# Performance work log

Hardware: AMD Instinct MI355X
Metric: run time of the kernel (lower is better)

## Reference

```python
import jax, jax.numpy as jnp
import numpy as np

N_GENES = 15135
K = int(np.ceil(0.5 * N_GENES))  # 7568, PyG TopKPooling ratio=0.5
BS, E, F_IN, H, HF, NC, L = 8, 242160, 64, 128, 512, 2, 3


def setup_inputs() -> dict:
    key = jax.random.key(0)
    ks = jax.random.split(key, 16)
    def lin(k, fin, fout):
        s = 1.0 / np.sqrt(fin)
        return jax.random.normal(k, (fin, fout), jnp.float32) * s
    x = jax.random.normal(ks[0], (BS, N_GENES, F_IN), jnp.float32)
    batch = jnp.zeros((BS,), jnp.int32)
    edge_index = jax.random.randint(ks[1], (2, E), 0, N_GENES, dtype=jnp.int32)
    CAT = L * H
    return {
        "x": x,
        "batch": batch,
        "edge_index": edge_index,
        "W1": lin(ks[2], F_IN, H), "b1": jnp.zeros((H,), jnp.float32),
        "W2": lin(ks[3], H, H),    "b2": jnp.zeros((H,), jnp.float32),
        "W3": lin(ks[4], H, H),    "b3": jnp.zeros((H,), jnp.float32),
        "topk_w": jax.random.normal(ks[5], (CAT,), jnp.float32) / np.sqrt(CAT),
        "fcW": lin(ks[6], CAT, 1), "fcb": jnp.zeros((1,), jnp.float32),
        "lin1W": lin(ks[7], K, HF), "lin1b": jnp.zeros((HF,), jnp.float32),
        "lin2W": lin(ks[8], HF, NC), "lin2b": jnp.zeros((NC,), jnp.float32),
    }


def reference(x, batch, edge_index, W1, b1, W2, b2, W3, b3,
              topk_w, fcW, fcb, lin1W, lin1b, lin2W, lin2b):
    bs = x.shape[0]
    # --- GCN normalization with self-loops (PyG GCNConv defaults) ---
    loop = jnp.arange(N_GENES, dtype=edge_index.dtype)
    src = jnp.concatenate([edge_index[0], loop])
    dst = jnp.concatenate([edge_index[1], loop])
    deg = jnp.zeros((N_GENES,), x.dtype).at[dst].add(1.0)
    dinv = jax.lax.rsqrt(deg)  # deg >= 1 due to self-loops
    norm = dinv[src] * dinv[dst]  # [E+N]

    def gcn(h, W, b):
        h = h @ W                                   # [bs, N, H]
        msg = h[:, src, :] * norm[None, :, None]    # gather + edge weight
        agg = jnp.zeros_like(h).at[:, dst, :].add(msg)  # scatter-add
        return agg + b

    h1 = jax.nn.relu(gcn(x, W1, b1))
    h2 = jax.nn.relu(gcn(h1, W2, b2))
    h3 = jax.nn.relu(gcn(h2, W3, b3))
    # mode='cat': stack on last dim then flatten -> feature order (H, layer)
    xc = jnp.stack([h1, h2, h3], -1).reshape(bs, N_GENES, -1)  # [bs, N, L*H]

    # --- TopKPooling (score = tanh(x.w/||w||), keep top ceil(0.5*N)) ---
    score = jnp.tanh((xc @ topk_w) / jnp.linalg.norm(topk_w))  # [bs, N]
    top_s, perm = jax.lax.top_k(score, K)                       # [bs, K]
    xp = jnp.take_along_axis(xc, perm[..., None], axis=1) * top_s[..., None]

    z = (xp @ fcW + fcb)[..., 0]          # [bs, K]
    h = jax.nn.relu(z @ lin1W + lin1b)    # [bs, HF]; dropout inactive (eval)
    logits = h @ lin2W + lin2b            # [bs, NC]
    return jax.nn.log_softmax(logits, axis=-1)
```

## Files before the change

kernel.cpp:

```cpp
#include <hip/hip_runtime.h>

#define N_G   15135
#define E_N   242160
#define BSZ   8
#define K_TOP 7568
#define NH    128
#define NBIN  65536
#define SUFS  65600

typedef float f4v __attribute__((ext_vector_type(4)));
typedef float f2v __attribute__((ext_vector_type(2)));

__global__ void zero_kernel(int* __restrict__ p, int n) {
  int i = blockIdx.x * 1024 + threadIdx.x;
  if (i < n) p[i] = 0;
}

__global__ void count_kernel(const int* __restrict__ ei, int* __restrict__ cnt) {
  int e = blockIdx.x * 256 + threadIdx.x;
  if (e < E_N) atomicAdd(&cnt[ei[E_N + e]], 1);
}

__global__ __launch_bounds__(1024) void scan_kernel(const int* __restrict__ cnt,
                                                    int* __restrict__ rowstart,
                                                    float* __restrict__ dinv,
                                                    int4* __restrict__ rowdesc,
                                                    int* __restrict__ gctr,
                                                    const float* __restrict__ topk_w,
                                                    float* __restrict__ scal) {
  __shared__ int buf[1024];
  __shared__ int base;
  int tid = threadIdx.x;
  int i = blockIdx.x * 1024 + tid;
  int v = (i < N_G) ? cnt[i] : 0;
  float di = 1.0f / sqrtf((float)(v + 1));
  if (i < N_G) dinv[i] = di;
  buf[tid] = v;
  __syncthreads();
  for (int s = 1; s < 1024; s <<= 1) {
    int t = (tid >= s) ? buf[tid - s] : 0;
    __syncthreads();
    buf[tid] += t;
    __syncthreads();
  }
  if (tid == 1023) base = atomicAdd(gctr, buf[1023]);
  __syncthreads();
  if (i < N_G) {
    int rs = base + buf[tid] - v;
    rowstart[i] = rs;
    rowdesc[i] = make_int4(rs, v, __float_as_int(di), 0);
  }
  if (blockIdx.x == 0) {
    __shared__ float fbuf[512];
    if (tid < 512) {
      float w = (tid < 384) ? topk_w[tid] : 0.f;
      fbuf[tid] = w * w;
    }
    __syncthreads();
    for (int s = 256; s > 0; s >>= 1) {
      if (tid < s) fbuf[tid] += fbuf[tid + s];
      __syncthreads();
    }
    if (tid == 0) scal[0] = 1.0f / sqrtf(fbuf[0]);
  }
}

__global__ void fill_kernel(const int* __restrict__ ei, const int* __restrict__ rowstart,
                            const float* __restrict__ dinv, int* __restrict__ fillc,
                            int2* __restrict__ csr) {
  int e = blockIdx.x * 256 + threadIdx.x;
  if (e < E_N) {
    int s = ei[e], d = ei[E_N + e];
    int pos = rowstart[d] + atomicAdd(&fillc[d], 1);
    csr[pos] = make_int2(s, __float_as_int(dinv[s]));
  }
}

template<int CIN, bool BR>
__global__ __launch_bounds__(256, 6) void mm_kernel(const float* __restrict__ A,
                                                    const float* __restrict__ W,
                                                    const float* __restrict__ bias,
                                                    float* __restrict__ out) {
  __shared__ float Bst[32][132];
  __shared__ float Ast2[32][68];
  int tid = threadIdx.x;
  int b = blockIdx.x & 7;
  int ib = blockIdx.x >> 3;
  int rb0 = b * N_G + ib * 64;
  int rmax = N_G - ib * 64;
  int c0 = (tid & 31) * 4;
  int r0 = (tid >> 5) * 8;
  float acc[8][4];
#pragma unroll
  for (int i = 0; i < 8; i++)
#pragma unroll
    for (int j = 0; j < 4; j++) acc[i][j] = 0.f;

  for (int k0 = 0; k0 < CIN; k0 += 32) {
    {
      int koff = (tid & 7) * 4;
      int row = tid >> 3;
#pragma unroll
      for (int p = 0; p < 2; ++p) {
        int r = row + p * 32;
        f4v v = {0.f, 0.f, 0.f, 0.f};
        if (r < rmax) v = __builtin_nontemporal_load((const f4v*)(A + (size_t)(rb0 + r) * CIN + k0 + koff));
        Ast2[koff + 0][r] = v.x; Ast2[koff + 1][r] = v.y;
        Ast2[koff + 2][r] = v.z; Ast2[koff + 3][r] = v.w;
      }
    }
    {
      int cc = (tid & 31) * 4;
      int kr = tid >> 5;
#pragma unroll
      for (int p = 0; p < 4; ++p) {
        int k = kr + p * 8;
        *(float4*)&Bst[k][cc] = *(const float4*)(W + (size_t)(k0 + k) * NH + cc);
      }
    }
    __syncthreads();
#pragma unroll 4
    for (int kk = 0; kk < 32; ++kk) {
      float a[8], bb[4];
      *(float4*)&a[0] = *(const float4*)&Ast2[kk][r0];
      *(float4*)&a[4] = *(const float4*)&Ast2[kk][r0 + 4];
      *(float4*)&bb[0] = *(const float4*)&Bst[kk][c0];
#pragma unroll
      for (int i = 0; i < 8; i++)
#pragma unroll
        for (int j = 0; j < 4; j++)
          acc[i][j] = fmaf(a[i], bb[j], acc[i][j]);
    }
    __syncthreads();
  }
  float b0 = 0.f, b1 = 0.f, b2 = 0.f, b3 = 0.f;
  if (BR) { b0 = bias[c0]; b1 = bias[c0+1]; b2 = bias[c0+2]; b3 = bias[c0+3]; }
#pragma unroll
  for (int i = 0; i < 8; i++) {
    int r = r0 + i;
    if (r < rmax) {
      float4 v;
      if (BR) {
        v.x = fmaxf(acc[i][0] + b0, 0.f); v.y = fmaxf(acc[i][1] + b1, 0.f);
        v.z = fmaxf(acc[i][2] + b2, 0.f); v.w = fmaxf(acc[i][3] + b3, 0.f);
      } else {
        v.x = acc[i][0]; v.y = acc[i][1]; v.z = acc[i][2]; v.w = acc[i][3];
      }
      *(float4*)(out + (size_t)(rb0 + r) * NH + c0) = v;
    }
  }
}

__global__ __launch_bounds__(256) void agg64_kernel(const float* __restrict__ src,
                                                    const int2* __restrict__ csr,
                                                    const int4* __restrict__ rowdesc,
                                                    float* __restrict__ dst) {
  int b = blockIdx.x & 7;
  int chunk = blockIdx.x >> 3;
  int wave = threadIdx.x >> 6, lane = threadIdx.x & 63;
  int d = chunk * 4 + wave;
  if (d >= N_G) return;
  d = __builtin_amdgcn_readfirstlane(d);
  int4 rd = rowdesc[d];
  int e0 = rd.x, n = rd.y;
  float dv = __int_as_float(rd.z);
  const float* sb = src + (size_t)b * N_G * 64;
  const int2* ce = csr + e0;
  float acc[8];
  acc[0] = dv * sb[(size_t)d * 64 + lane];
#pragma unroll
  for (int k = 1; k < 8; ++k) acc[k] = 0.f;
  int l = 0;
  if (n >= 8) {
    int2 pA[8]; float vA[8];
#pragma unroll
    for (int k = 0; k < 8; ++k) pA[k] = ce[k];
#pragma unroll
    for (int k = 0; k < 8; ++k) vA[k] = sb[(size_t)pA[k].x * 64 + lane];
    l = 8;
    for (; l + 8 <= n; l += 8) {
      int2 pB[8]; float vB[8];
#pragma unroll
      for (int k = 0; k < 8; ++k) pB[k] = ce[l + k];
#pragma unroll
      for (int k = 0; k < 8; ++k) vB[k] = sb[(size_t)pB[k].x * 64 + lane];
#pragma unroll
      for (int k = 0; k < 8; ++k) acc[k] = fmaf(__int_as_float(pA[k].y), vA[k], acc[k]);
#pragma unroll
      for (int k = 0; k < 8; ++k) { pA[k] = pB[k]; vA[k] = vB[k]; }
    }
#pragma unroll
    for (int k = 0; k < 8; ++k) acc[k] = fmaf(__int_as_float(pA[k].y), vA[k], acc[k]);
  }
  for (; l < n; ++l) {
    int2 p = ce[l];
    acc[0] = fmaf(__int_as_float(p.y), sb[(size_t)p.x * 64 + lane], acc[0]);
  }
  float s = ((acc[0] + acc[1]) + (acc[2] + acc[3])) + ((acc[4] + acc[5]) + (acc[6] + acc[7]));
  __builtin_nontemporal_store(dv * s, &dst[((size_t)b * N_G + d) * 64 + lane]);
}

template<int CH0>
__global__ __launch_bounds__(256) void agg_h_kernel(const float* __restrict__ hw,
                                                    const int2* __restrict__ csr,
                                                    const int4* __restrict__ rowdesc,
                                                    const float* __restrict__ bias,
                                                    float* __restrict__ hout) {
  int b = blockIdx.x & 7;
  int chunk = blockIdx.x >> 3;
  int wave = threadIdx.x >> 6, lane = threadIdx.x & 63;
  int d0 = chunk * 8 + wave * 2;
  if (d0 >= N_G) return;
  d0 = __builtin_amdgcn_readfirstlane(d0);
  int d1i = d0 + 1;
  int has1 = (d1i < N_G);
  int dB = has1 ? d1i : d0;
  int4 rdA = rowdesc[d0];
  int4 rdB = rowdesc[dB];
  int nA = rdA.y, nB = has1 ? rdB.y : 0;
  float dvA = __int_as_float(rdA.z);
  float dvB = __int_as_float(rdB.z);
  const float* sb = hw + (size_t)b * N_G * NH + CH0 + lane;
  const int2* ceA = csr + rdA.x;
  const int2* ceB = csr + rdB.x;
  float axA[4], axB[4];
  axA[0] = dvA * sb[(size_t)d0 * NH];
  axB[0] = has1 ? dvB * sb[(size_t)dB * NH] : 0.f;
#pragma unroll
  for (int k = 1; k < 4; ++k) { axA[k] = 0.f; axB[k] = 0.f; }
  int lA = 0, lB = 0;
  while (lA + 8 <= nA && lB + 8 <= nB) {
    int2 pA[8], pB[8]; float vA[8], vB[8];
#pragma unroll
    for (int k = 0; k < 8; ++k) pA[k] = ceA[lA + k];
#pragma unroll
    for (int k = 0; k < 8; ++k) pB[k] = ceB[lB + k];
#pragma unroll
    for (int k = 0; k < 8; ++k) vA[k] = sb[(size_t)pA[k].x * NH];
#pragma unroll
    for (int k = 0; k < 8; ++k) vB[k] = sb[(size_t)pB[k].x * NH];
#pragma unroll
    for (int k = 0; k < 8; ++k) axA[k & 3] = fmaf(__int_as_float(pA[k].y), vA[k], axA[k & 3]);
#pragma unroll
    for (int k = 0; k < 8; ++k) axB[k & 3] = fmaf(__int_as_float(pB[k].y), vB[k], axB[k & 3]);
    lA += 8; lB += 8;
  }
  for (; lA + 8 <= nA; lA += 8) {
    int2 pA[8]; float vA[8];
#pragma unroll
    for (int k = 0; k < 8; ++k) pA[k] = ceA[lA + k];
#pragma unroll
    for (int k = 0; k < 8; ++k) vA[k] = sb[(size_t)pA[k].x * NH];
#pragma unroll
    for (int k = 0; k < 8; ++k) axA[k & 3] = fmaf(__int_as_float(pA[k].y), vA[k], axA[k & 3]);
  }
  for (; lB + 8 <= nB; lB += 8) {
    int2 pB[8]; float vB[8];
#pragma unroll
    for (int k = 0; k < 8; ++k) pB[k] = ceB[lB + k];
#pragma unroll
    for (int k = 0; k < 8; ++k) vB[k] = sb[(size_t)pB[k].x * NH];
#pragma unroll
    for (int k = 0; k < 8; ++k) axB[k & 3] = fmaf(__int_as_float(pB[k].y), vB[k], axB[k & 3]);
  }
  for (; lA < nA; ++lA) {
    int2 p = ceA[lA];
    axA[0] = fmaf(__int_as_float(p.y), sb[(size_t)p.x * NH], axA[0]);
  }
  for (; lB < nB; ++lB) {
    int2 p = ceB[lB];
    axB[0] = fmaf(__int_as_float(p.y), sb[(size_t)p.x * NH], axB[0]);
  }
  float bb = bias[CH0 + lane];
  {
    float s = (axA[0] + axA[1]) + (axA[2] + axA[3]);
    __builtin_nontemporal_store(fmaxf(fmaf(dvA, s, bb), 0.f),
        &hout[((size_t)b * N_G + d0) * NH + CH0 + lane]);
  }
  if (has1) {
    float s = (axB[0] + axB[1]) + (axB[2] + axB[3]);
    __builtin_nontemporal_store(fmaxf(fmaf(dvB, s, bb), 0.f),
        &hout[((size_t)b * N_G + d1i) * NH + CH0 + lane]);
  }
}

template<int CH0, bool FINAL>
__global__ __launch_bounds__(256) void agg_score_h_kernel(const float* __restrict__ hw,
                                                          const int2* __restrict__ csr,
                                                          const int4* __restrict__ rowdesc,
                                                          const float* __restrict__ bias,
                                                          const float* __restrict__ h1,
                                                          const float* __restrict__ h2,
                                                          const float* __restrict__ topk_w,
                                                          const float* __restrict__ fcW,
                                                          const float* __restrict__ scal,
                                                          float* __restrict__ score,
                                                          float* __restrict__ d2a,
                                                          unsigned* __restrict__ keys,
                                                          int* __restrict__ hist,
                                                          float2* __restrict__ dpart) {
  int b = blockIdx.x & 7;
  int chunk = blockIdx.x >> 3;
  int wave = threadIdx.x >> 6, lane = threadIdx.x & 63;
  int d0 = chunk * 8 + wave * 2;
  if (d0 >= N_G) return;
  d0 = __builtin_amdgcn_readfirstlane(d0);
  int d1i = d0 + 1;
  int has1 = (d1i < N_G);
  int dB = has1 ? d1i : d0;
  int4 rdA = rowdesc[d0];
  int4 rdB = rowdesc[dB];
  int nA = rdA.y, nB = has1 ? rdB.y : 0;
  float dvA = __int_as_float(rdA.z);
  float dvB = __int_as_float(rdB.z);
  const float* sb = hw + (size_t)b * N_G * NH + CH0 + lane;
  const int2* ceA = csr + rdA.x;
  const int2* ceB = csr + rdB.x;
  size_t rbA = ((size_t)b * N_G + d0) * NH + CH0 + lane;
  size_t rbB = ((size_t)b * N_G + dB) * NH + CH0 + lane;
  float u1A = __builtin_nontemporal_load(&h1[rbA]);
  float u2A = __builtin_nontemporal_load(&h2[rbA]);
  float u1B = __builtin_nontemporal_load(&h1[rbB]);
  float u2B = __builtin_nontemporal_load(&h2[rbB]);
  float axA[4], axB[4];
  axA[0] = dvA * sb[(size_t)d0 * NH];
  axB[0] = has1 ? dvB * sb[(size_t)dB * NH] : 0.f;
#pragma unroll
  for (int k = 1; k < 4; ++k) { axA[k] = 0.f; axB[k] = 0.f; }
  int lA = 0, lB = 0;
  while (lA + 8 <= nA && lB + 8 <= nB) {
    int2 pA[8], pB[8]; float vA[8], vB[8];
#pragma unroll
    for (int k = 0; k < 8; ++k) pA[k] = ceA[lA + k];
#pragma unroll
    for (int k = 0; k < 8; ++k) pB[k] = ceB[lB + k];
#pragma unroll
    for (int k = 0; k < 8; ++k) vA[k] = sb[(size_t)pA[k].x * NH];
#pragma unroll
    for (int k = 0; k < 8; ++k) vB[k] = sb[(size_t)pB[k].x * NH];
#pragma unroll
    for (int k = 0; k < 8; ++k) axA[k & 3] = fmaf(__int_as_float(pA[k].y), vA[k], axA[k & 3]);
#pragma unroll
    for (int k = 0; k < 8; ++k) axB[k & 3] = fmaf(__int_as_float(pB[k].y), vB[k], axB[k & 3]);
    lA += 8; lB += 8;
  }
  for (; lA + 8 <= nA; lA += 8) {
    int2 pA[8]; float vA[8];
#pragma unroll
    for (int k = 0; k < 8; ++k) pA[k] = ceA[lA + k];
#pragma unroll
    for (int k = 0; k < 8; ++k) vA[k] = sb[(size_t)pA[k].x * NH];
#pragma unroll
    for (int k = 0; k < 8; ++k) axA[k & 3] = fmaf(__int_as_float(pA[k].y), vA[k], axA[k & 3]);
  }
  for (; lB + 8 <= nB; lB += 8) {
    int2 pB[8]; float vB[8];
#pragma unroll
    for (int k = 0; k < 8; ++k) pB[k] = ceB[lB + k];
#pragma unroll
    for (int k = 0; k < 8; ++k) vB[k] = sb[(size_t)pB[k].x * NH];
#pragma unroll
    for (int k = 0; k < 8; ++k) axB[k & 3] = fmaf(__int_as_float(pB[k].y), vB[k], axB[k & 3]);
  }
  for (; lA < nA; ++lA) {
    int2 p = ceA[lA];
    axA[0] = fmaf(__int_as_float(p.y), sb[(size_t)p.x * NH], axA[0]);
  }
  for (; lB < nB; ++lB) {
    int2 p = ceB[lB];
    axB[0] = fmaf(__int_as_float(p.y), sb[(size_t)p.x * NH], axB[0]);
  }
  float bb = bias[CH0 + lane];
  float rA = fmaxf(fmaf(dvA, (axA[0] + axA[1]) + (axA[2] + axA[3]), bb), 0.f);
  float rB = fmaxf(fmaf(dvB, (axB[0] + axB[1]) + (axB[2] + axB[3]), bb), 0.f);
  int ch3 = (CH0 + lane) * 3;
  float t0 = topk_w[ch3 + 0], t1 = topk_w[ch3 + 1], t2 = topk_w[ch3 + 2];
  float f0 = fcW[ch3 + 0],  f1 = fcW[ch3 + 1],  f2 = fcW[ch3 + 2];
  float d1A = u1A * t0 + u2A * t1 + rA * t2;
  float d2A = u1A * f0 + u2A * f1 + rA * f2;
  float d1B = u1B * t0 + u2B * t1 + rB * t2;
  float d2B = u1B * f0 + u2B * f1 + rB * f2;
#pragma unroll
  for (int sh = 32; sh > 0; sh >>= 1) {
    d1A += __shfl_down(d1A, sh);
    d2A += __shfl_down(d2A, sh);
    d1B += __shfl_down(d1B, sh);
    d2B += __shfl_down(d2B, sh);
  }
  if (lane == 0) {
    int gwA = b * N_G + d0;
    if (!FINAL) {
      dpart[gwA] = make_float2(d1A, d2A);
      if (has1) dpart[gwA + 1] = make_float2(d1B, d2B);
    } else {
      float sc0 = scal[0];
      {
        float2 pp = dpart[gwA];
        float D1 = pp.x + d1A, D2 = pp.y + d2A;
        float sc = tanhf(D1 * sc0);
        score[gwA] = sc;
        d2a[gwA] = D2;
        unsigned u = __float_as_uint(sc);
        unsigned k32 = (u & 0x80000000u) ? ~u : (u | 0x80000000u);
        keys[gwA] = k32;
        atomicAdd(&hist[b * NBIN + (int)(k32 >> 16)], 1);
      }
      if (has1) {
        int gwB = gwA + 1;
        float2 pp = dpart[gwB];
        float D1 = pp.x + d1B, D2 = pp.y + d2B;
        float sc = tanhf(D1 * sc0);
        score[gwB] = sc;
        d2a[gwB] = D2;
        unsigned u = __float_as_uint(sc);
        unsigned k32 = (u & 0x80000000u) ? ~u : (u | 0x80000000u);
        keys[gwB] = k32;
        atomicAdd(&hist[b * NBIN + (int)(k32 >> 16)], 1);
      }
    }
  }
}

__global__ __launch_bounds__(1024) void suffix_kernel(const int* __restrict__ hist,
                                                      int* __restrict__ suf) {
  __shared__ int buf[1024];
  int b = blockIdx.x;
  const int* hb = hist + b * NBIN;
  int* sb = suf + b * SUFS;
  int t = threadIdx.x;
  int base = t * 64;
  int s = 0;
  for (int k = 0; k < 64; ++k) s += hb[base + k];
  buf[t] = s;
  __syncthreads();
  for (int off = 1; off < 1024; off <<= 1) {
    int v = (t + off < 1024) ? buf[t + off] : 0;
    __syncthreads();
    buf[t] += v;
    __syncthreads();
  }
  int acc = buf[t] - s;
  if (t == 0) sb[NBIN] = 0;
  for (int k = 63; k >= 0; --k) {
    acc += hb[base + k];
    sb[base + k] = acc;
  }
}

__global__ void scatter_kernel(const unsigned* __restrict__ keys, int* __restrict__ hist,
                               const int* __restrict__ suf, int2* __restrict__ bucket) {
  int b = blockIdx.y;
  int i = blockIdx.x * 256 + threadIdx.x;
  if (i >= N_G) return;
  unsigned k = keys[b * N_G + i];
  int bin = (int)(k >> 16);
  int old = atomicSub(&hist[b * NBIN + bin], 1);
  int pos = suf[b * SUFS + bin + 1] + old - 1;
  bucket[b * N_G + pos] = make_int2((int)k, i);
}

__global__ void rank_z_kernel(const unsigned* __restrict__ keys, const int* __restrict__ suf,
                              const int2* __restrict__ bucket, const float* __restrict__ score,
                              const float* __restrict__ d2a, const float* __restrict__ fcb,
                              float* __restrict__ z) {
  int b = blockIdx.y;
  int i = blockIdx.x * 256 + threadIdx.x;
  if (i >= N_G) return;
  int gw = b * N_G + i;
  unsigned k = keys[gw];
  int bin = (int)(k >> 16);
  int lo = suf[b * SUFS + bin + 1];
  int hi = suf[b * SUFS + bin];
  int r = lo;
  const int2* bk = bucket + b * N_G;
  for (int p = lo; p < hi; ++p) {
    int2 e = bk[p];
    unsigned kj = (unsigned)e.x;
    r += (kj > k || (kj == k && e.y < i)) ? 1 : 0;
  }
  if (r < K_TOP) z[b * K_TOP + r] = fmaf(score[gw], d2a[gw], fcb[0]);
}

__global__ __launch_bounds__(256) void lin1_kernel(const float* __restrict__ z,
                                                   const float* __restrict__ W,
                                                   float* __restrict__ hpre) {
  __shared__ float zb[237];
  int b = blockIdx.y, rs = blockIdx.x;
  int r0 = rs * 237;
  int rn = K_TOP - r0; if (rn > 237) rn = 237;
  for (int q = threadIdx.x; q < rn; q += 256) zb[q] = z[b * K_TOP + r0 + q];
  __syncthreads();
  int c = threadIdx.x;
  float a0 = 0.f, a1 = 0.f;
  for (int r = 0; r < rn; ++r) {
    float zz = zb[r];
    const float* wr = W + (size_t)(r0 + r) * 512;
    a0 = fmaf(zz, wr[c], a0);
    a1 = fmaf(zz, wr[c + 256], a1);
  }
  atomicAdd(&hpre[b * 512 + c], a0);
  atomicAdd(&hpre[b * 512 + c + 256], a1);
}

__global__ __launch_bounds__(128) void lin2_kernel(const float* __restrict__ hpre,
                                                   const float* __restrict__ l1b,
                                                   const float* __restrict__ W2,
                                                   const float* __restrict__ l2b,
                                                   float* __restrict__ out) {
  int b = blockIdx.x, tid = threadIdx.x;
  float a0 = 0.f, a1 = 0.f;
  for (int j = tid; j < 512; j += 128) {
    float t = fmaxf(hpre[b * 512 + j] + l1b[j], 0.f);
    a0 = fmaf(t, W2[j * 2 + 0], a0);
    a1 = fmaf(t, W2[j * 2 + 1], a1);
  }
#pragma unroll
  for (int s = 32; s > 0; s >>= 1) {
    a0 += __shfl_down(a0, s);
    a1 += __shfl_down(a1, s);
  }
  __shared__ float red[2][2];
  if ((tid & 63) == 0) { red[tid >> 6][0] = a0; red[tid >> 6][1] = a1; }
  __syncthreads();
  if (tid == 0) {
    float l0 = red[0][0] + red[1][0] + l2b[0];
    float l1 = red[0][1] + red[1][1] + l2b[1];
    float m = fmaxf(l0, l1);
    float lse = m + logf(expf(l0 - m) + expf(l1 - m));
    out[b * 2 + 0] = l0 - lse;
    out[b * 2 + 1] = l1 - lse;
  }
}

extern "C" void kernel_launch(void* const* d_in, const int* in_sizes, int n_in,
                              void* d_out, int out_size, void* d_ws, size_t ws_size,
                              hipStream_t stream) {
  const float* x   = (const float*)d_in[0];
  const int*   ei  = (const int*)d_in[2];
  const float* W1  = (const float*)d_in[3];
  const float* b1  = (const float*)d_in[4];
  const float* W2  = (const float*)d_in[5];
  const float* b2  = (const float*)d_in[6];
  const float* W3  = (const float*)d_in[7];
  const float* b3  = (const float*)d_in[8];
  const float* tkw = (const float*)d_in[9];
  const float* fcW = (const float*)d_in[10];
  const float* fcb = (const float*)d_in[11];
  const float* l1W = (const float*)d_in[12];
  const float* l1b = (const float*)d_in[13];
  const float* l2W = (const float*)d_in[14];
  const float* l2b = (const float*)d_in[15];
  float* out = (float*)d_out;

  char* ws = (char*)d_ws;
  size_t off = 0;
  auto alloc = [&](size_t bytes) {
    char* p = ws + off;
    off += (bytes + 255) & ~(size_t)255;
    return p;
  };
  int*   cnt   = (int*)alloc(15136 * 4);
  int*   fillc = (int*)alloc(15136 * 4);
  int*   gctr  = (int*)alloc(256);
  float* hpre  = (float*)alloc(4096 * 4);
  int*   hist  = (int*)alloc((size_t)BSZ * NBIN * 4);
  int*   rowstart = (int*)alloc(15136 * 4);
  float* dinv  = (float*)alloc(15136 * 4);
  int4*  rowdesc = (int4*)alloc(15136 * 16);
  float* scal  = (float*)alloc(64);
  float* z     = (float*)alloc((size_t)BSZ * K_TOP * 4);
  float* score = (float*)alloc(121088 * 4);
  float* d2a   = (float*)alloc(121088 * 4);
  unsigned* keys = (unsigned*)alloc(121088 * 4);
  int*   suf   = (int*)alloc((size_t)BSZ * SUFS * 4);
  int2*  bucket = (int2*)alloc(121088 * 8);
  int2*  csr   = (int2*)alloc((size_t)E_N * 8);
  float* ax = (float*)alloc((size_t)BSZ * N_G * 64 * 4);
  float* hw = (float*)alloc((size_t)BSZ * N_G * NH * 4);
  float* h1 = (float*)alloc((size_t)BSZ * N_G * NH * 4);
  float* h2 = (float*)alloc((size_t)BSZ * N_G * NH * 4);
  (void)ws_size; (void)in_sizes; (void)n_in; (void)out_size;

  float2* dpart = (float2*)bucket;

  int zero_n = (int)(((char*)rowstart - (char*)cnt) / 4);
  zero_kernel<<<(zero_n + 1023) / 1024, 1024, 0, stream>>>(cnt, zero_n);
  count_kernel<<<(E_N + 255) / 256, 256, 0, stream>>>(ei, cnt);
  scan_kernel<<<(N_G + 1023) / 1024, 1024, 0, stream>>>(cnt, rowstart, dinv, rowdesc, gctr, tkw, scal);
  fill_kernel<<<(E_N + 255) / 256, 256, 0, stream>>>(ei, rowstart, dinv, fillc, csr);

  dim3 mmg(8 * 237);
  int aggblocks  = 8 * ((N_G + 3) / 4);
  int aggblocks2 = 8 * ((N_G + 7) / 8);

  agg64_kernel<<<aggblocks, 256, 0, stream>>>(x, csr, rowdesc, ax);
  mm_kernel<64, true><<<mmg, 256, 0, stream>>>(ax, W1, b1, h1);
  mm_kernel<128, false><<<mmg, 256, 0, stream>>>(h1, W2, nullptr, hw);
  agg_h_kernel<0><<<aggblocks2, 256, 0, stream>>>(hw, csr, rowdesc, b2, h2);
  agg_h_kernel<64><<<aggblocks2, 256, 0, stream>>>(hw, csr, rowdesc, b2, h2);
  mm_kernel<128, false><<<mmg, 256, 0, stream>>>(h2, W3, nullptr, hw);
  agg_score_h_kernel<0, false><<<aggblocks2, 256, 0, stream>>>(hw, csr, rowdesc, b3, h1, h2,
                                                               tkw, fcW, scal, score, d2a,
                                                               keys, hist, dpart);
  agg_score_h_kernel<64, true><<<aggblocks2, 256, 0, stream>>>(hw, csr, rowdesc, b3, h1, h2,
                                                               tkw, fcW, scal, score, d2a,
                                                               keys, hist, dpart);

  dim3 ng((N_G + 255) / 256, BSZ);
  suffix_kernel<<<BSZ, 1024, 0, stream>>>(hist, suf);
  scatter_kernel<<<ng, 256, 0, stream>>>(keys, hist, suf, bucket);
  rank_z_kernel<<<ng, 256, 0, stream>>>(keys, suf, bucket, score, d2a, fcb, z);

  dim3 l1g(32, BSZ);
  lin1_kernel<<<l1g, 256, 0, stream>>>(z, l1W, hpre);
  lin2_kernel<<<BSZ, 128, 0, stream>>>(hpre, l1b, l2W, l2b, out);
}
```

Measured before the change: 638.7 us.

## Replace per-row gather kernels with edge-streaming multi-row aggregation kernel

Replaces the three aggregation kernels, which gave each wave one or two destination rows, with one templated kernel. In it each wave walks the contiguous CSR edge range of 32 consecutive rows and finalizes each row when the edge index crosses its bound. The aim is to remove load imbalance and tail inefficiency from short or uneven row degrees, and to keep an 8-deep prefetch pipeline of edges and gathered values running across row boundaries. The trade-offs are serialized finalize logic per row inside the wave, fewer waves in total (about 474 per batch), and scalar bound-checking inside the inner loop, which may reduce parallelism and latency hiding.

```diff
diff --git a/kernel.cpp b/kernel.cpp
--- a/kernel.cpp
+++ b/kernel.cpp
@@ -10,6 +10,7 @@
 
 typedef float f4v __attribute__((ext_vector_type(4)));
 typedef float f2v __attribute__((ext_vector_type(2)));
+typedef int   i2v __attribute__((ext_vector_type(2)));
 
 __global__ void zero_kernel(int* __restrict__ p, int n) {
   int i = blockIdx.x * 1024 + threadIdx.x;
@@ -151,273 +152,181 @@
   }
 }
 
-__global__ __launch_bounds__(256) void agg64_kernel(const float* __restrict__ src,
-                                                    const int2* __restrict__ csr,
-                                                    const int4* __restrict__ rowdesc,
-                                                    float* __restrict__ dst) {
+template<int NHS, int CH0, int MODE>
+__global__ __launch_bounds__(256) void stream_agg_kernel(
+    const float* __restrict__ table,
+    const int2* __restrict__ csr,
+    const int4* __restrict__ rowdesc,
+    const float* __restrict__ bias,
+    const float* __restrict__ h1,
+    const float* __restrict__ h2,
+    const float* __restrict__ topk_w,
+    const float* __restrict__ fcW,
+    const float* __restrict__ scal,
+    float* __restrict__ outp,
+    float2* __restrict__ dpart,
+    float* __restrict__ score,
+    float* __restrict__ d2a,
+    unsigned* __restrict__ keys,
+    int* __restrict__ hist) {
+  constexpr int R = 32;
   int b = blockIdx.x & 7;
-  int chunk = blockIdx.x >> 3;
-  int wave = threadIdx.x >> 6, lane = threadIdx.x & 63;
-  int d = chunk * 4 + wave;
-  if (d >= N_G) return;
-  d = __builtin_amdgcn_readfirstlane(d);
-  int4 rd = rowdesc[d];
-  int e0 = rd.x, n = rd.y;
-  float dv = __int_as_float(rd.z);
-  const float* sb = src + (size_t)b * N_G * 64;
-  const int2* ce = csr + e0;
-  float acc[8];
-  acc[0] = dv * sb[(size_t)d * 64 + lane];
-#pragma unroll
-  for (int k = 1; k < 8; ++k) acc[k] = 0.f;
-  int l = 0;
-  if (n >= 8) {
-    int2 pA[8]; float vA[8];
-#pragma unroll
-    for (int k = 0; k < 8; ++k) pA[k] = ce[k];
-#pragma unroll
-    for (int k = 0; k < 8; ++k) vA[k] = sb[(size_t)pA[k].x * 64 + lane];
-    l = 8;
-    for (; l + 8 <= n; l += 8) {
-      int2 pB[8]; float vB[8];
-#pragma unroll
-      for (int k = 0; k < 8; ++k) pB[k] = ce[l + k];
-#pragma unroll
-      for (int k = 0; k < 8; ++k) vB[k] = sb[(size_t)pB[k].x * 64 + lane];
-#pragma unroll
-      for (int k = 0; k < 8; ++k) acc[k] = fmaf(__int_as_float(pA[k].y), vA[k], acc[k]);
-#pragma unroll
-      for (int k = 0; k < 8; ++k) { pA[k] = pB[k]; vA[k] = vB[k]; }
-    }
-#pragma unroll
-    for (int k = 0; k < 8; ++k) acc[k] = fmaf(__int_as_float(pA[k].y), vA[k], acc[k]);
-  }
-  for (; l < n; ++l) {
-    int2 p = ce[l];
-    acc[0] = fmaf(__int_as_float(p.y), sb[(size_t)p.x * 64 + lane], acc[0]);
-  }
-  float s = ((acc[0] + acc[1]) + (acc[2] + acc[3])) + ((acc[4] + acc[5]) + (acc[6] + acc[7]));
-  __builtin_nontemporal_store(dv * s, &dst[((size_t)b * N_G + d) * 64 + lane]);
-}
-
-template<int CH0>
-__global__ __launch_bounds__(256) void agg_h_kernel(const float* __restrict__ hw,
-                                                    const int2* __restrict__ csr,
-                                                    const int4* __restrict__ rowdesc,
-                                                    const float* __restrict__ bias,
-                                                    float* __restrict__ hout) {
-  int b = blockIdx.x & 7;
-  int chunk = blockIdx.x >> 3;
-  int wave = threadIdx.x >> 6, lane = threadIdx.x & 63;
-  int d0 = chunk * 8 + wave * 2;
+  int wid = (blockIdx.x >> 3) * 4 + (threadIdx.x >> 6);
+  int lane = threadIdx.x & 63;
+  int d0 = wid * R;
   if (d0 >= N_G) return;
   d0 = __builtin_amdgcn_readfirstlane(d0);
-  int d1i = d0 + 1;
-  int has1 = (d1i < N_G);
-  int dB = has1 ? d1i : d0;
-  int4 rdA = rowdesc[d0];
-  int4 rdB = rowdesc[dB];
-  int nA = rdA.y, nB = has1 ? rdB.y : 0;
-  float dvA = __int_as_float(rdA.z);
-  float dvB = __int_as_float(rdB.z);
-  const float* sb = hw + (size_t)b * N_G * NH + CH0 + lane;
-  const int2* ceA = csr + rdA.x;
-  const int2* ceB = csr + rdB.x;
-  float axA[4], axB[4];
-  axA[0] = dvA * sb[(size_t)d0 * NH];
-  axB[0] = has1 ? dvB * sb[(size_t)dB * NH] : 0.f;
-#pragma unroll
-  for (int k = 1; k < 4; ++k) { axA[k] = 0.f; axB[k] = 0.f; }
-  int lA = 0, lB = 0;
-  while (lA + 8 <= nA && lB + 8 <= nB) {
-    int2 pA[8], pB[8]; float vA[8], vB[8];
-#pragma unroll
-    for (int k = 0; k < 8; ++k) pA[k] = ceA[lA + k];
-#pragma unroll
-    for (int k = 0; k < 8; ++k) pB[k] = ceB[lB + k];
-#pragma unroll
-    for (int k = 0; k < 8; ++k) vA[k] = sb[(size_t)pA[k].x * NH];
-#pragma unroll
-    for (int k = 0; k < 8; ++k) vB[k] = sb[(size_t)pB[k].x * NH];
-#pragma unroll
-    for (int k = 0; k < 8; ++k) axA[k & 3] = fmaf(__int_as_float(pA[k].y), vA[k], axA[k & 3]);
-#pragma unroll
-    for (int k = 0; k < 8; ++k) axB[k & 3] = fmaf(__int_as_float(pB[k].y), vB[k], axB[k & 3]);
-    lA += 8; lB += 8;
-  }
-  for (; lA + 8 <= nA; lA += 8) {
-    int2 pA[8]; float vA[8];
-#pragma unroll
-    for (int k = 0; k < 8; ++k) pA[k] = ceA[lA + k];
-#pragma unroll
-    for (int k = 0; k < 8; ++k) vA[k] = sb[(size_t)pA[k].x * NH];
-#pragma unroll
-    for (int k = 0; k < 8; ++k) axA[k & 3] = fmaf(__int_as_float(pA[k].y), vA[k], axA[k & 3]);
-  }
-  for (; lB + 8 <= nB; lB += 8) {
-    int2 pB[8]; float vB[8];
-#pragma unroll
-    for (int k = 0; k < 8; ++k) pB[k] = ceB[lB + k];
-#pragma unroll
-    for (int k = 0; k < 8; ++k) vB[k] = sb[(size_t)pB[k].x * NH];
-#pragma unroll
-    for (int k = 0; k < 8; ++k) axB[k & 3] = fmaf(__int_as_float(pB[k].y), vB[k], axB[k & 3]);
-  }
-  for (; lA < nA; ++lA) {
-    int2 p = ceA[lA];
-    axA[0] = fmaf(__int_as_float(p.y), sb[(size_t)p.x * NH], axA[0]);
-  }
-  for (; lB < nB; ++lB) {
-    int2 p = ceB[lB];
-    axB[0] = fmaf(__int_as_float(p.y), sb[(size_t)p.x * NH], axB[0]);
-  }
-  float bb = bias[CH0 + lane];
-  {
-    float s = (axA[0] + axA[1]) + (axA[2] + axA[3]);
-    __builtin_nontemporal_store(fmaxf(fmaf(dvA, s, bb), 0.f),
-        &hout[((size_t)b * N_G + d0) * NH + CH0 + lane]);
-  }
-  if (has1) {
-    float s = (axB[0] + axB[1]) + (axB[2] + axB[3]);
-    __builtin_nontemporal_store(fmaxf(fmaf(dvB, s, bb), 0.f),
-        &hout[((size_t)b * N_G + d1i) * NH + CH0 + lane]);
-  }
-}
-
-template<int CH0, bool FINAL>
-__global__ __launch_bounds__(256) void agg_score_h_kernel(const float* __restrict__ hw,
-                                                          const int2* __restrict__ csr,
-                                                          const int4* __restrict__ rowdesc,
-                                                          const float* __restrict__ bias,
-                                                          const float* __restrict__ h1,
-                                                          const float* __restrict__ h2,
-                                                          const float* __restrict__ topk_w,
-                                                          const float* __restrict__ fcW,
-                                                          const float* __restrict__ scal,
-                                                          float* __restrict__ score,
-                                                          float* __restrict__ d2a,
-                                                          unsigned* __restrict__ keys,
-                                                          int* __restrict__ hist,
-                                                          float2* __restrict__ dpart) {
-  int b = blockIdx.x & 7;
-  int chunk = blockIdx.x >> 3;
-  int wave = threadIdx.x >> 6, lane = threadIdx.x & 63;
-  int d0 = chunk * 8 + wave * 2;
-  if (d0 >= N_G) return;
-  d0 = __builtin_amdgcn_readfirstlane(d0);
-  int d1i = d0 + 1;
-  int has1 = (d1i < N_G);
-  int dB = has1 ? d1i : d0;
-  int4 rdA = rowdesc[d0];
-  int4 rdB = rowdesc[dB];
-  int nA = rdA.y, nB = has1 ? rdB.y : 0;
-  float dvA = __int_as_float(rdA.z);
-  float dvB = __int_as_float(rdB.z);
-  const float* sb = hw + (size_t)b * N_G * NH + CH0 + lane;
-  const int2* ceA = csr + rdA.x;
-  const int2* ceB = csr + rdB.x;
-  size_t rbA = ((size_t)b * N_G + d0) * NH + CH0 + lane;
-  size_t rbB = ((size_t)b * N_G + dB) * NH + CH0 + lane;
-  float u1A = __builtin_nontemporal_load(&h1[rbA]);
-  float u2A = __builtin_nontemporal_load(&h2[rbA]);
-  float u1B = __builtin_nontemporal_load(&h1[rbB]);
-  float u2B = __builtin_nontemporal_load(&h2[rbB]);
-  float axA[4], axB[4];
-  axA[0] = dvA * sb[(size_t)d0 * NH];
-  axB[0] = has1 ? dvB * sb[(size_t)dB * NH] : 0.f;
-#pragma unroll
-  for (int k = 1; k < 4; ++k) { axA[k] = 0.f; axB[k] = 0.f; }
-  int lA = 0, lB = 0;
-  while (lA + 8 <= nA && lB + 8 <= nB) {
-    int2 pA[8], pB[8]; float vA[8], vB[8];
-#pragma unroll
-    for (int k = 0; k < 8; ++k) pA[k] = ceA[lA + k];
-#pragma unroll
-    for (int k = 0; k < 8; ++k) pB[k] = ceB[lB + k];
-#pragma unroll
-    for (int k = 0; k < 8; ++k) vA[k] = sb[(size_t)pA[k].x * NH];
-#pragma unroll
-    for (int k = 0; k < 8; ++k) vB[k] = sb[(size_t)pB[k].x * NH];
-#pragma unroll
-    for (int k = 0; k < 8; ++k) axA[k & 3] = fmaf(__int_as_float(pA[k].y), vA[k], axA[k & 3]);
-#pragma unroll
-    for (int k = 0; k < 8; ++k) axB[k & 3] = fmaf(__int_as_float(pB[k].y), vB[k], axB[k & 3]);
-    lA += 8; lB += 8;
-  }
-  for (; lA + 8 <= nA; lA += 8) {
-    int2 pA[8]; float vA[8];
-#pragma unroll
-    for (int k = 0; k < 8; ++k) pA[k] = ceA[lA + k];
-#pragma unroll
-    for (int k = 0; k < 8; ++k) vA[k] = sb[(size_t)pA[k].x * NH];
-#pragma unroll
-    for (int k = 0; k < 8; ++k) axA[k & 3] = fmaf(__int_as_float(pA[k].y), vA[k], axA[k & 3]);
-  }
-  for (; lB + 8 <= nB; lB += 8) {
-    int2 pB[8]; float vB[8];
-#pragma unroll
-    for (int k = 0; k < 8; ++k) pB[k] = ceB[lB + k];
-#pragma unroll
-    for (int k = 0; k < 8; ++k) vB[k] = sb[(size_t)pB[k].x * NH];
-#pragma unroll
-    for (int k = 0; k < 8; ++k) axB[k & 3] = fmaf(__int_as_float(pB[k].y), vB[k], axB[k & 3]);
-  }
-  for (; lA < nA; ++lA) {
-    int2 p = ceA[lA];
-    axA[0] = fmaf(__int_as_float(p.y), sb[(size_t)p.x * NH], axA[0]);
-  }
-  for (; lB < nB; ++lB) {
-    int2 p = ceB[lB];
-    axB[0] = fmaf(__int_as_float(p.y), sb[(size_t)p.x * NH], axB[0]);
-  }
-  float bb = bias[CH0 + lane];
-  float rA = fmaxf(fmaf(dvA, (axA[0] + axA[1]) + (axA[2] + axA[3]), bb), 0.f);
-  float rB = fmaxf(fmaf(dvB, (axB[0] + axB[1]) + (axB[2] + axB[3]), bb), 0.f);
-  int ch3 = (CH0 + lane) * 3;
-  float t0 = topk_w[ch3 + 0], t1 = topk_w[ch3 + 1], t2 = topk_w[ch3 + 2];
-  float f0 = fcW[ch3 + 0],  f1 = fcW[ch3 + 1],  f2 = fcW[ch3 + 2];
-  float d1A = u1A * t0 + u2A * t1 + rA * t2;
-  float d2A = u1A * f0 + u2A * f1 + rA * f2;
-  float d1B = u1B * t0 + u2B * t1 + rB * t2;
-  float d2B = u1B * f0 + u2B * f1 + rB * f2;
-#pragma unroll
-  for (int sh = 32; sh > 0; sh >>= 1) {
-    d1A += __shfl_down(d1A, sh);
-    d2A += __shfl_down(d2A, sh);
-    d1B += __shfl_down(d1B, sh);
-    d2B += __shfl_down(d2B, sh);
-  }
-  if (lane == 0) {
-    int gwA = b * N_G + d0;
-    if (!FINAL) {
-      dpart[gwA] = make_float2(d1A, d2A);
-      if (has1) dpart[gwA + 1] = make_float2(d1B, d2B);
+  int nrows = N_G - d0; if (nrows > R) nrows = R;
+
+  int rl = (lane < nrows) ? lane : (nrows - 1);
+  int4 rdl = rowdesc[d0 + rl];
+  int boundv = rdl.x + rdl.y;
+  float dinvv = __int_as_float(rdl.z);
+
+  const float* sb0 = table + (size_t)b * N_G * NHS + CH0;
+  const i2v* csrv = (const i2v*)csr;
+
+  int e    = __builtin_amdgcn_readfirstlane(__shfl(rdl.x, 0));
+  int eEnd = __builtin_amdgcn_readfirstlane(__shfl(boundv, nrows - 1));
+  int r = 0;
+  int bound = __builtin_amdgcn_readfirstlane(__shfl(boundv, 0));
+  float dv = __shfl(dinvv, 0);
+  float acc = 0.f;
+
+  float selfC, selfN;
+  selfC = sb0[(size_t)d0 * NHS + lane];
+  { int dn = d0 + 1; if (dn >= N_G) dn = N_G - 1; selfN = sb0[(size_t)dn * NHS + lane]; }
+
+  float bb = 0.f;
+  if constexpr (MODE >= 1) bb = bias[CH0 + lane];
+
+  float u1C = 0.f, u1N = 0.f, u2C = 0.f, u2N = 0.f;
+  float t0 = 0.f, t1 = 0.f, t2 = 0.f, f0 = 0.f, f1 = 0.f, f2 = 0.f;
+  float sc0 = 0.f;
+  float2 dpC = make_float2(0.f, 0.f), dpN = make_float2(0.f, 0.f);
+  if constexpr (MODE >= 2) {
+    size_t rb = ((size_t)b * N_G + d0) * NHS + CH0 + lane;
+    u1C = __builtin_nontemporal_load(&h1[rb]);
+    u2C = __builtin_nontemporal_load(&h2[rb]);
+    int dn = d0 + 1; if (dn >= N_G) dn = N_G - 1;
+    size_t rb1 = ((size_t)b * N_G + dn) * NHS + CH0 + lane;
+    u1N = __builtin_nontemporal_load(&h1[rb1]);
+    u2N = __builtin_nontemporal_load(&h2[rb1]);
+    int ch3 = (CH0 + lane) * 3;
+    t0 = topk_w[ch3]; t1 = topk_w[ch3 + 1]; t2 = topk_w[ch3 + 2];
+    f0 = fcW[ch3];    f1 = fcW[ch3 + 1];    f2 = fcW[ch3 + 2];
+  }
+  if constexpr (MODE == 3) {
+    sc0 = scal[0];
+    dpC = dpart[b * N_G + d0];
+    { int dn = d0 + 1; if (dn >= N_G) dn = N_G - 1; dpN = dpart[b * N_G + dn]; }
+  }
+
+  auto finalize = [&]() {
+    float s = acc + dv * selfC;
+    acc = 0.f;
+    int d = d0 + r;
+    selfC = selfN;
+    { int dn = d + 2; if (dn >= N_G) dn = N_G - 1; selfN = sb0[(size_t)dn * NHS + lane]; }
+    if constexpr (MODE == 0) {
+      __builtin_nontemporal_store(dv * s, &outp[((size_t)b * N_G + d) * NHS + CH0 + lane]);
+    } else if constexpr (MODE == 1) {
+      float rr = fmaxf(fmaf(dv, s, bb), 0.f);
+      __builtin_nontemporal_store(rr, &outp[((size_t)b * N_G + d) * NHS + CH0 + lane]);
     } else {
-      float sc0 = scal[0];
-      {
-        float2 pp = dpart[gwA];
-        float D1 = pp.x + d1A, D2 = pp.y + d2A;
-        float sc = tanhf(D1 * sc0);
-        score[gwA] = sc;
-        d2a[gwA] = D2;
-        unsigned u = __float_as_uint(sc);
-        unsigned k32 = (u & 0x80000000u) ? ~u : (u | 0x80000000u);
-        keys[gwA] = k32;
-        atomicAdd(&hist[b * NBIN + (int)(k32 >> 16)], 1);
-      }
-      if (has1) {
-        int gwB = gwA + 1;
-        float2 pp = dpart[gwB];
-        float D1 = pp.x + d1B, D2 = pp.y + d2B;
-        float sc = tanhf(D1 * sc0);
-        score[gwB] = sc;
-        d2a[gwB] = D2;
-        unsigned u = __float_as_uint(sc);
-        unsigned k32 = (u & 0x80000000u) ? ~u : (u | 0x80000000u);
-        keys[gwB] = k32;
-        atomicAdd(&hist[b * NBIN + (int)(k32 >> 16)], 1);
-      }
-    }
+      float rx = fmaxf(fmaf(dv, s, bb), 0.f);
+      float d1 = u1C * t0 + u2C * t1 + rx * t2;
+      float d2 = u1C * f0 + u2C * f1 + rx * f2;
+      u1C = u1N; u2C = u2N;
+      { int dn = d + 2; if (dn >= N_G) dn = N_G - 1;
+        size_t rb = ((size_t)b * N_G + dn) * NHS + CH0 + lane;
+        u1N = __builtin_nontemporal_load(&h1[rb]);
+        u2N = __builtin_nontemporal_load(&h2[rb]); }
+#pragma unroll
+      for (int sh = 32; sh > 0; sh >>= 1) {
+        d1 += __shfl_down(d1, sh);
+        d2 += __shfl_down(d2, sh);
+      }
+      int gw = b * N_G + d;
+      if constexpr (MODE == 2) {
+        if (lane == 0) dpart[gw] = make_float2(d1, d2);
+      } else {
+        float2 pp = dpC;
+        dpC = dpN;
+        { int dn = d + 2; if (dn >= N_G) dn = N_G - 1; dpN = dpart[b * N_G + dn]; }
+        if (lane == 0) {
+          float D1 = pp.x + d1, D2 = pp.y + d2;
+          float scv = tanhf(D1 * sc0);
+          score[gw] = scv;
+          d2a[gw] = D2;
+          unsigned u = __float_as_uint(scv);
+          unsigned k32 = (u & 0x80000000u) ? ~u : (u | 0x80000000u);
+          keys[gw] = k32;
+          atomicAdd(&hist[b * NBIN + (int)(k32 >> 16)], 1);
+        }
+      }
+    }
+  };
+
+  i2v csn[8];
+  float wC[8], vC[8];
+#pragma unroll
+  for (int k = 0; k < 8; ++k) {
+    int ei = e + k; if (ei > E_N - 1) ei = E_N - 1;
+    csn[k] = __builtin_nontemporal_load(&csrv[ei]);
+  }
+#pragma unroll
+  for (int k = 0; k < 8; ++k) {
+    int s = __builtin_amdgcn_readfirstlane(csn[k][0]);
+    wC[k] = __uint_as_float((unsigned)__builtin_amdgcn_readfirstlane(csn[k][1]));
+    vC[k] = sb0[(size_t)s * NHS + lane];
+  }
+#pragma unroll
+  for (int k = 0; k < 8; ++k) {
+    int ei = e + 8 + k; if (ei > E_N - 1) ei = E_N - 1;
+    csn[k] = __builtin_nontemporal_load(&csrv[ei]);
+  }
+
+  while (e < eEnd) {
+    bool more = (e + 8 < eEnd);
+    float wN[8], vN[8];
+    if (more) {
+#pragma unroll
+      for (int k = 0; k < 8; ++k) {
+        int s = __builtin_amdgcn_readfirstlane(csn[k][0]);
+        wN[k] = __uint_as_float((unsigned)__builtin_amdgcn_readfirstlane(csn[k][1]));
+        vN[k] = sb0[(size_t)s * NHS + lane];
+      }
+#pragma unroll
+      for (int k = 0; k < 8; ++k) {
+        int ei = e + 16 + k; if (ei > E_N - 1) ei = E_N - 1;
+        csn[k] = __builtin_nontemporal_load(&csrv[ei]);
+      }
+    }
+    int lim = eEnd - e; if (lim > 8) lim = 8;
+#pragma unroll
+    for (int k = 0; k < 8; ++k) {
+      if (k < lim) {
+        int eg = e + k;
+        while (eg == bound) {
+          finalize();
+          ++r;
+          int rr2 = (r < nrows) ? r : (nrows - 1);
+          bound = __builtin_amdgcn_readfirstlane(__shfl(boundv, rr2));
+          dv = __shfl(dinvv, rr2);
+        }
+        acc = fmaf(wC[k], vC[k], acc);
+      }
+    }
+#pragma unroll
+    for (int k = 0; k < 8; ++k) { wC[k] = wN[k]; vC[k] = vN[k]; }
+    e += 8;
+  }
+
+  while (r < nrows) {
+    dv = __shfl(dinvv, r);
+    finalize();
+    ++r;
   }
 }
 
@@ -590,21 +499,27 @@
   fill_kernel<<<(E_N + 255) / 256, 256, 0, stream>>>(ei, rowstart, dinv, fillc, csr);
 
   dim3 mmg(8 * 237);
-  int aggblocks  = 8 * ((N_G + 3) / 4);
-  int aggblocks2 = 8 * ((N_G + 7) / 8);
-
-  agg64_kernel<<<aggblocks, 256, 0, stream>>>(x, csr, rowdesc, ax);
+  int nwid = (N_G + 31) / 32;
+  int sgrid = 8 * ((nwid + 3) / 4);
+
+  stream_agg_kernel<64, 0, 0><<<sgrid, 256, 0, stream>>>(
+      x, csr, rowdesc, nullptr, nullptr, nullptr, nullptr, nullptr, nullptr,
+      ax, nullptr, nullptr, nullptr, nullptr, nullptr);
   mm_kernel<64, true><<<mmg, 256, 0, stream>>>(ax, W1, b1, h1);
   mm_kernel<128, false><<<mmg, 256, 0, stream>>>(h1, W2, nullptr, hw);
-  agg_h_kernel<0><<<aggblocks2, 256, 0, stream>>>(hw, csr, rowdesc, b2, h2);
-  agg_h_kernel<64><<<aggblocks2, 256, 0, stream>>>(hw, csr, rowdesc, b2, h2);
+  stream_agg_kernel<128, 0, 1><<<sgrid, 256, 0, stream>>>(
+      hw, csr, rowdesc, b2, nullptr, nullptr, nullptr, nullptr, nullptr,
+      h2, nullptr, nullptr, nullptr, nullptr, nullptr);
+  stream_agg_kernel<128, 64, 1><<<sgrid, 256, 0, stream>>>(
+      hw, csr, rowdesc, b2, nullptr, nullptr, nullptr, nullptr, nullptr,
+      h2, nullptr, nullptr, nullptr, nullptr, nullptr);
   mm_kernel<128, false><<<mmg, 256, 0, stream>>>(h2, W3, nullptr, hw);
-  agg_score_h_kernel<0, false><<<aggblocks2, 256, 0, stream>>>(hw, csr, rowdesc, b3, h1, h2,
-                                                               tkw, fcW, scal, score, d2a,
-                                                               keys, hist, dpart);
-  agg_score_h_kernel<64, true><<<aggblocks2, 256, 0, stream>>>(hw, csr, rowdesc, b3, h1, h2,
-                                                               tkw, fcW, scal, score, d2a,
-                                                               keys, hist, dpart);
+  stream_agg_kernel<128, 0, 2><<<sgrid, 256, 0, stream>>>(
+      hw, csr, rowdesc, b3, h1, h2, tkw, fcW, scal,
+      nullptr, dpart, score, d2a, keys, hist);
+  stream_agg_kernel<128, 64, 3><<<sgrid, 256, 0, stream>>>(
+      hw, csr, rowdesc, b3, h1, h2, tkw, fcW, scal,
+      nullptr, dpart, score, d2a, keys, hist);
 
   dim3 ng((N_G + 255) / 256, BSZ);
   suffix_kernel<<<BSZ, 1024, 0, stream>>>(hist, suf);
```

After: 804.4 us. +25.9%, slower.
